# Performance work log

Measured on AMD Instinct MI355X. Metric: run time of the kernel, lower is better.

The kernel has to match this reference:

```python
import jax, jax.numpy as jnp
import numpy as np
from jax import lax

B, T, D, H = 256, 1024, 64, 100


def setup_inputs() -> dict:
    key = jax.random.key(0)
    ks = jax.random.split(key, 8)
    s = 1.0 / np.sqrt(H)  # PyTorch LSTM/Linear init scale
    x = jax.random.normal(ks[0], (B, T, D), dtype=jnp.float32)
    h0 = jnp.zeros((1, B, H), dtype=jnp.float32)
    c0 = jnp.zeros((1, B, H), dtype=jnp.float32)
    # PyTorch gate order: i, f, g, o stacked along first dim (4H)
    W_ih = jax.random.uniform(ks[1], (4 * H, D), jnp.float32, -s, s)
    W_hh = jax.random.uniform(ks[2], (4 * H, H), jnp.float32, -s, s)
    b_ih = jax.random.uniform(ks[3], (4 * H,), jnp.float32, -s, s)
    b_hh = jax.random.uniform(ks[4], (4 * H,), jnp.float32, -s, s)
    W_fc = jax.random.uniform(ks[5], (1, H), jnp.float32, -s, s)
    b_fc = jax.random.uniform(ks[6], (1,), jnp.float32, -s, s)
    return {"x": x, "h0": h0, "c0": c0, "W_ih": W_ih, "W_hh": W_hh,
            "b_ih": b_ih, "b_hh": b_hh, "W_fc": W_fc, "b_fc": b_fc}


def reference(x, h0, c0, W_ih, W_hh, b_ih, b_hh, W_fc, b_fc):
    # Precompute input contribution to all gates in one big GEMM: [B,T,4H]
    xg = jnp.einsum('btd,gd->btg', x, W_ih) + (b_ih + b_hh)

    def step(carry, xt):  # xt: [B,4H]
        h, c = carry
        gates = xt + h @ W_hh.T
        i, f, g, o = jnp.split(gates, 4, axis=-1)
        i = jax.nn.sigmoid(i)
        f = jax.nn.sigmoid(f)
        g = jnp.tanh(g)
        o = jax.nn.sigmoid(o)
        c = f * c + i * g
        h = o * jnp.tanh(c)
        return (h, c), None

    (h_T, _), _ = lax.scan(step, (h0[0], c0[0]), jnp.swapaxes(xg, 0, 1))
    # dropout is identity in eval mode; fc head on final hidden state
    out = h_T @ W_fc.T + b_fc  # [B, 1]
    return out
```

## Files before the change

### kernel.cpp

```cpp
#include <hip/hip_runtime.h>
#include <math.h>

#define BATCH 256
#define TSTEPS 1024
#define DIN 64
#define HID 100
#define GATES 400
#define BLOCK 512
#define XT 32

__global__ __launch_bounds__(BLOCK, 2)
void lstm_fused_kernel(const float* __restrict__ x, const float* __restrict__ h0,
                       const float* __restrict__ c0, const float* __restrict__ W_ih,
                       const float* __restrict__ W_hh, const float* __restrict__ b_ih,
                       const float* __restrict__ b_hh, const float* __restrict__ W_fc,
                       const float* __restrict__ b_fc, float* __restrict__ out)
{
    __shared__ __align__(16) float h_buf[2][104];
    __shared__ __align__(16) float x_tile[XT * DIN];
    __shared__ float red[128];

    const int tid = threadIdx.x;
    const int b = blockIdx.x;
    const int q = tid & 3;
    const int n = tid >> 2;
    const bool gate_thread = (tid < GATES);
    const int g = q * HID + n;

    float wih[DIN];
    float whh[HID];
    float bias = 0.f;
    if (gate_thread) {
        const float4* wi4 = reinterpret_cast<const float4*>(W_ih + g * DIN);
        #pragma unroll
        for (int k = 0; k < DIN / 4; ++k) {
            float4 v = wi4[k];
            wih[4*k+0] = v.x; wih[4*k+1] = v.y; wih[4*k+2] = v.z; wih[4*k+3] = v.w;
        }
        const float4* wh4 = reinterpret_cast<const float4*>(W_hh + g * HID);
        #pragma unroll
        for (int k = 0; k < HID / 4; ++k) {
            float4 v = wh4[k];
            whh[4*k+0] = v.x; whh[4*k+1] = v.y; whh[4*k+2] = v.z; whh[4*k+3] = v.w;
        }
        bias = b_ih[g] + b_hh[g];
    }

    if (tid < HID) h_buf[0][tid] = h0[b * HID + tid];
    float c = 0.f;
    if (gate_thread && q == 0) c = c0[b * HID + n];
    __syncthreads();

    for (int t = 0; t < TSTEPS; ++t) {
        if ((t & (XT - 1)) == 0) {
            const float4* xs = reinterpret_cast<const float4*>(
                x + (size_t)b * TSTEPS * DIN + (size_t)t * DIN);
            reinterpret_cast<float4*>(x_tile)[tid] = xs[tid];
            __syncthreads();
        }
        const int cur = t & 1, nxt = cur ^ 1;

        if (gate_thread) {
            float a0 = 0.f, a1 = 0.f, a2 = 0.f, a3 = 0.f;
            const float4* h4 = reinterpret_cast<const float4*>(h_buf[cur]);
            #pragma unroll
            for (int k = 0; k < HID / 4; ++k) {
                float4 hv = h4[k];
                a0 += hv.x * whh[4*k+0];
                a1 += hv.y * whh[4*k+1];
                a2 += hv.z * whh[4*k+2];
                a3 += hv.w * whh[4*k+3];
            }
            const float4* x4 = reinterpret_cast<const float4*>(&x_tile[(t & (XT - 1)) * DIN]);
            #pragma unroll
            for (int k = 0; k < DIN / 4; ++k) {
                float4 xv = x4[k];
                a0 += xv.x * wih[4*k+0];
                a1 += xv.y * wih[4*k+1];
                a2 += xv.z * wih[4*k+2];
                a3 += xv.w * wih[4*k+3];
            }
            float z = ((a0 + a1) + (a2 + a3)) + bias;

            float zq = (q == 2) ? 2.f * z : z;
            float e = __expf(-zq);
            float s = 1.f / (1.f + e);
            float a = (q == 2) ? (2.f * s - 1.f) : s;

            float fv = __shfl_down(a, 1);
            float gv = __shfl_down(a, 2);
            float ov = __shfl_down(a, 3);
            if (q == 0) {
                c = fv * c + a * gv;
                float e2 = __expf(-2.f * c);
                float th = 2.f / (1.f + e2) - 1.f;
                h_buf[nxt][n] = ov * th;
            }
        }
        __syncthreads();
    }

    if (tid < HID) red[tid] = h_buf[TSTEPS & 1][tid] * W_fc[tid];
    __syncthreads();
    if (tid == 0) {
        float s = 0.f;
        #pragma unroll 4
        for (int i = 0; i < HID; ++i) s += red[i];
        out[b] = s + b_fc[0];
    }
}

extern "C" void kernel_launch(void* const* d_in, const int* in_sizes, int n_in,
                              void* d_out, int out_size, void* d_ws, size_t ws_size,
                              hipStream_t stream) {
    const float* x    = (const float*)d_in[0];
    const float* h0   = (const float*)d_in[1];
    const float* c0   = (const float*)d_in[2];
    const float* W_ih = (const float*)d_in[3];
    const float* W_hh = (const float*)d_in[4];
    const float* b_ih = (const float*)d_in[5];
    const float* b_hh = (const float*)d_in[6];
    const float* W_fc = (const float*)d_in[7];
    const float* b_fc = (const float*)d_in[8];
    float* out = (float*)d_out;

    lstm_fused_kernel<<<dim3(BATCH), dim3(BLOCK), 0, stream>>>(
        x, h0, c0, W_ih, W_hh, b_ih, b_hh, W_fc, b_fc, out);
}
```

Measured before the change: 1.119 ms.

## Rewrite LSTM recurrence as bf16 MFMA over 16-sequence batch tiles

```diff
diff --git a/kernel.cpp b/kernel.cpp
--- a/kernel.cpp
+++ b/kernel.cpp
@@ -1,112 +1,174 @@
 #include <hip/hip_runtime.h>
+#include <hip/hip_bf16.h>
 #include <math.h>
 
 #define BATCH 256
 #define TSTEPS 1024
 #define DIN 64
 #define HID 100
-#define GATES 400
-#define BLOCK 512
-#define XT 32
+#define MB 16
+#define NWG (BATCH / MB)
+#define WAVES 7
+#define BLOCK (WAVES * 64)
+#define TPW 4
+#define HROW 136
+#define L2E 1.4426950408889634f
 
-__global__ __launch_bounds__(BLOCK, 2)
-void lstm_fused_kernel(const float* __restrict__ x, const float* __restrict__ h0,
-                       const float* __restrict__ c0, const float* __restrict__ W_ih,
-                       const float* __restrict__ W_hh, const float* __restrict__ b_ih,
-                       const float* __restrict__ b_hh, const float* __restrict__ W_fc,
-                       const float* __restrict__ b_fc, float* __restrict__ out)
+typedef __attribute__((ext_vector_type(8))) short bf16x8;
+typedef __attribute__((ext_vector_type(4))) float f32x4;
+
+__device__ __forceinline__ short f2bf(float f) {
+    return (short)__bfloat16_as_ushort(__float2bfloat16(f));
+}
+__device__ __forceinline__ float x2f(float x) {
+#if __has_builtin(__builtin_amdgcn_exp2f)
+    return __builtin_amdgcn_exp2f(x);
+#else
+    return exp2f(x);
+#endif
+}
+__device__ __forceinline__ float rcpf_(float x) { return __builtin_amdgcn_rcpf(x); }
+
+__global__ __launch_bounds__(BLOCK, 1)
+void lstm_mfma_kernel(const float* __restrict__ x, const float* __restrict__ h0,
+                      const float* __restrict__ c0, const float* __restrict__ W_ih,
+                      const float* __restrict__ W_hh, const float* __restrict__ b_ih,
+                      const float* __restrict__ b_hh, const float* __restrict__ W_fc,
+                      const float* __restrict__ b_fc, float* __restrict__ out)
 {
-    __shared__ __align__(16) float h_buf[2][104];
-    __shared__ __align__(16) float x_tile[XT * DIN];
-    __shared__ float red[128];
+    __shared__ short Hl[MB * HROW];
+    __shared__ float red[WAVES * 4][MB];
 
     const int tid = threadIdx.x;
-    const int b = blockIdx.x;
-    const int q = tid & 3;
-    const int n = tid >> 2;
-    const bool gate_thread = (tid < GATES);
-    const int g = q * HID + n;
+    const int w   = tid >> 6;
+    const int l   = tid & 63;
+    const int lb  = l & 15;
+    const int lg  = l >> 4;
+    const int bg0 = blockIdx.x * MB;
 
-    float wih[DIN];
-    float whh[HID];
-    float bias = 0.f;
-    if (gate_thread) {
-        const float4* wi4 = reinterpret_cast<const float4*>(W_ih + g * DIN);
+    bf16x8 Ah[TPW][4];
+    bf16x8 Ax[TPW][2];
+    f32x4  bias[TPW];
+    float  cc[TPW];
+    int    uc[TPW];
+    #pragma unroll
+    for (int ti = 0; ti < TPW; ++ti) {
+        const int tg = w * TPW + ti;
+        const int R  = tg * 16 + lb;
+        const int u  = R >> 2;
+        const int qg = R & 3;
+        const bool val = (u < HID);
+        const float scl = (qg == 2) ? 2.0f * L2E : -L2E;
+        const float* wr  = W_hh + (size_t)(qg * HID + (val ? u : 0)) * HID;
+        const float* wr2 = W_ih + (size_t)(qg * HID + (val ? u : 0)) * DIN;
         #pragma unroll
-        for (int k = 0; k < DIN / 4; ++k) {
-            float4 v = wi4[k];
-            wih[4*k+0] = v.x; wih[4*k+1] = v.y; wih[4*k+2] = v.z; wih[4*k+3] = v.w;
+        for (int kt = 0; kt < 4; ++kt)
+            #pragma unroll
+            for (int j = 0; j < 8; ++j) {
+                int k = kt * 32 + lg * 8 + j;
+                float v = (val && k < HID) ? wr[k] : 0.f;
+                Ah[ti][kt][j] = f2bf(v * scl);
+            }
+        #pragma unroll
+        for (int kt = 0; kt < 2; ++kt)
+            #pragma unroll
+            for (int j = 0; j < 8; ++j) {
+                float v = val ? wr2[kt * 32 + lg * 8 + j] : 0.f;
+                Ax[ti][kt][j] = f2bf(v * scl);
+            }
+        const int u_c = tg * 4 + lg;
+        uc[ti] = u_c;
+        const bool vcv = (u_c < HID);
+        f32x4 bb;
+        #pragma unroll
+        for (int r = 0; r < 4; ++r) {
+            float s2 = (r == 2) ? 2.0f * L2E : -L2E;
+            bb[r] = vcv ? (b_ih[r * HID + u_c] + b_hh[r * HID + u_c]) * s2 : 0.f;
         }
-        const float4* wh4 = reinterpret_cast<const float4*>(W_hh + g * HID);
-        #pragma unroll
-        for (int k = 0; k < HID / 4; ++k) {
-            float4 v = wh4[k];
-            whh[4*k+0] = v.x; whh[4*k+1] = v.y; whh[4*k+2] = v.z; whh[4*k+3] = v.w;
-        }
-        bias = b_ih[g] + b_hh[g];
+        bias[ti] = bb;
+        cc[ti] = vcv ? c0[(size_t)(bg0 + lb) * HID + u_c] : 0.f;
     }
 
-    if (tid < HID) h_buf[0][tid] = h0[b * HID + tid];
-    float c = 0.f;
-    if (gate_thread && q == 0) c = c0[b * HID + n];
+    for (int idx = tid; idx < MB * 128; idx += BLOCK) {
+        int bb2 = idx >> 7, k = idx & 127;
+        float v = (k < HID) ? h0[(size_t)(bg0 + bb2) * HID + k] : 0.f;
+        Hl[bb2 * HROW + k] = f2bf(v);
+    }
     __syncthreads();
 
+    const float* xp = x + (size_t)(bg0 + lb) * TSTEPS * DIN + lg * 8;
+    const short* hb = Hl + lb * HROW + lg * 8;
+    short*       hw = Hl + lb * HROW;
+
+    float hlast[TPW];
+    #pragma unroll
+    for (int ti = 0; ti < TPW; ++ti) hlast[ti] = 0.f;
+
     for (int t = 0; t < TSTEPS; ++t) {
-        if ((t & (XT - 1)) == 0) {
-            const float4* xs = reinterpret_cast<const float4*>(
-                x + (size_t)b * TSTEPS * DIN + (size_t)t * DIN);
-            reinterpret_cast<float4*>(x_tile)[tid] = xs[tid];
-            __syncthreads();
+        bf16x8 Bh0 = *(const bf16x8*)(hb);
+        bf16x8 Bh1 = *(const bf16x8*)(hb + 32);
+        bf16x8 Bh2 = *(const bf16x8*)(hb + 64);
+        bf16x8 Bh3 = *(const bf16x8*)(hb + 96);
+        __syncthreads();
+
+        const float4* p0 = (const float4*)(xp + (size_t)t * DIN);
+        const float4* p1 = (const float4*)(xp + (size_t)t * DIN + 32);
+        float4 va = p0[0];
+        float4 vb = p0[1];
+        float4 vc4 = p1[0];
+        float4 vd = p1[1];
+
+        f32x4 acc[TPW];
+        #pragma unroll
+        for (int ti = 0; ti < TPW; ++ti) acc[ti] = bias[ti];
+        #pragma unroll
+        for (int ti = 0; ti < TPW; ++ti) {
+            acc[ti] = __builtin_amdgcn_mfma_f32_16x16x32_bf16(Ah[ti][0], Bh0, acc[ti], 0, 0, 0);
+            acc[ti] = __builtin_amdgcn_mfma_f32_16x16x32_bf16(Ah[ti][1], Bh1, acc[ti], 0, 0, 0);
+            acc[ti] = __builtin_amdgcn_mfma_f32_16x16x32_bf16(Ah[ti][2], Bh2, acc[ti], 0, 0, 0);
+            acc[ti] = __builtin_amdgcn_mfma_f32_16x16x32_bf16(Ah[ti][3], Bh3, acc[ti], 0, 0, 0);
         }
-        const int cur = t & 1, nxt = cur ^ 1;
+        bf16x8 Bx0, Bx1;
+        Bx0[0]=f2bf(va.x); Bx0[1]=f2bf(va.y); Bx0[2]=f2bf(va.z); Bx0[3]=f2bf(va.w);
+        Bx0[4]=f2bf(vb.x); Bx0[5]=f2bf(vb.y); Bx0[6]=f2bf(vb.z); Bx0[7]=f2bf(vb.w);
+        Bx1[0]=f2bf(vc4.x); Bx1[1]=f2bf(vc4.y); Bx1[2]=f2bf(vc4.z); Bx1[3]=f2bf(vc4.w);
+        Bx1[4]=f2bf(vd.x); Bx1[5]=f2bf(vd.y); Bx1[6]=f2bf(vd.z); Bx1[7]=f2bf(vd.w);
+        #pragma unroll
+        for (int ti = 0; ti < TPW; ++ti) {
+            acc[ti] = __builtin_amdgcn_mfma_f32_16x16x32_bf16(Ax[ti][0], Bx0, acc[ti], 0, 0, 0);
+            acc[ti] = __builtin_amdgcn_mfma_f32_16x16x32_bf16(Ax[ti][1], Bx1, acc[ti], 0, 0, 0);
+        }
 
-        if (gate_thread) {
-            float a0 = 0.f, a1 = 0.f, a2 = 0.f, a3 = 0.f;
-            const float4* h4 = reinterpret_cast<const float4*>(h_buf[cur]);
-            #pragma unroll
-            for (int k = 0; k < HID / 4; ++k) {
-                float4 hv = h4[k];
-                a0 += hv.x * whh[4*k+0];
-                a1 += hv.y * whh[4*k+1];
-                a2 += hv.z * whh[4*k+2];
-                a3 += hv.w * whh[4*k+3];
-            }
-            const float4* x4 = reinterpret_cast<const float4*>(&x_tile[(t & (XT - 1)) * DIN]);
-            #pragma unroll
-            for (int k = 0; k < DIN / 4; ++k) {
-                float4 xv = x4[k];
-                a0 += xv.x * wih[4*k+0];
-                a1 += xv.y * wih[4*k+1];
-                a2 += xv.z * wih[4*k+2];
-                a3 += xv.w * wih[4*k+3];
-            }
-            float z = ((a0 + a1) + (a2 + a3)) + bias;
-
-            float zq = (q == 2) ? 2.f * z : z;
-            float e = __expf(-zq);
-            float s = 1.f / (1.f + e);
-            float a = (q == 2) ? (2.f * s - 1.f) : s;
-
-            float fv = __shfl_down(a, 1);
-            float gv = __shfl_down(a, 2);
-            float ov = __shfl_down(a, 3);
-            if (q == 0) {
-                c = fv * c + a * gv;
-                float e2 = __expf(-2.f * c);
-                float th = 2.f / (1.f + e2) - 1.f;
-                h_buf[nxt][n] = ov * th;
-            }
+        #pragma unroll
+        for (int ti = 0; ti < TPW; ++ti) {
+            float Ei = x2f(acc[ti][0]);
+            float Ef = x2f(acc[ti][1]);
+            float G  = x2f(acc[ti][2]);
+            float Eo = x2f(acc[ti][3]);
+            float P  = (1.f + Ei) * (1.f + G);
+            float D  = (1.f + Ef) * P;
+            float num = fmaf(cc[ti], P, (G - 1.f) * (1.f + Ef));
+            float c2  = num * rcpf_(D);
+            cc[ti] = c2;
+            float C2 = x2f(fminf(c2, 15.f) * (2.0f * L2E));
+            float hv = (C2 - 1.f) * rcpf_((1.f + Eo) * (C2 + 1.f));
+            hlast[ti] = hv;
+            if (uc[ti] < HID) hw[uc[ti]] = f2bf(hv);
         }
         __syncthreads();
     }
 
-    if (tid < HID) red[tid] = h_buf[TSTEPS & 1][tid] * W_fc[tid];
+    float part = 0.f;
+    #pragma unroll
+    for (int ti = 0; ti < TPW; ++ti)
+        if (uc[ti] < HID) part += hlast[ti] * W_fc[uc[ti]];
+    red[w * 4 + lg][lb] = part;
     __syncthreads();
-    if (tid == 0) {
-        float s = 0.f;
-        #pragma unroll 4
-        for (int i = 0; i < HID; ++i) s += red[i];
-        out[b] = s + b_fc[0];
+    if (tid < MB) {
+        float s = b_fc[0];
+        #pragma unroll
+        for (int i = 0; i < WAVES * 4; ++i) s += red[i][tid];
+        out[bg0 + tid] = s;
     }
 }
 
@@ -124,6 +186,6 @@
     const float* b_fc = (const float*)d_in[8];
     float* out = (float*)d_out;
 
-    lstm_fused_kernel<<<dim3(BATCH), dim3(BLOCK), 0, stream>>>(
+    lstm_mfma_kernel<<<dim3(NWG), dim3(BLOCK), 0, stream>>>(
         x, h0, c0, W_ih, W_hh, b_ih, b_hh, W_fc, b_fc, out);
 }
```

Result: slower. 2.183 ms (+95.0%).
